# Kernel tuning notes

Measured on AMD Instinct MI355X. Metric: run time of the kernel, lower is better.

Reference implementation:

```python
import jax, jax.numpy as jnp
import numpy as np

N_NODES = 50000
N_EDGES = 640000
N_GRAPHS = 64
IN_DIM, HID, OUT_DIM = 128, 256, 4


def gcn_conv(x, src, dst, W, b, n_nodes):
    """PyG GCNConv: linear transform, then sym-normalized aggregation with self-loops."""
    h = x @ W  # [N, out]
    deg = jnp.zeros((n_nodes,), h.dtype).at[dst].add(1.0) + 1.0  # +1 self-loop
    dinv = jax.lax.rsqrt(deg)  # deg >= 1 always
    norm = dinv[src] * dinv[dst]  # [E]
    msg = h[src] * norm[:, None]  # [E, out]  gather + scale
    agg = jax.ops.segment_sum(msg, dst, num_segments=n_nodes)  # scatter-add
    agg = agg + h * (dinv * dinv)[:, None]  # self-loop contribution
    return agg + b


def global_mean_pool(x, batch, num_graphs):
    s = jax.ops.segment_sum(x, batch, num_segments=num_graphs)
    cnt = jax.ops.segment_sum(jnp.ones((x.shape[0],), x.dtype), batch, num_segments=num_graphs)
    return s / jnp.clip(cnt, 1.0)[:, None]


def setup_inputs() -> dict:
    key = jax.random.key(0)
    ks = jax.random.split(key, 8)
    x = jax.random.normal(ks[0], (N_NODES, IN_DIM), jnp.float32)
    src = jax.random.randint(ks[1], (N_EDGES,), 0, N_NODES, jnp.int64 if jax.config.jax_enable_x64 else jnp.int32)
    dst = jax.random.randint(ks[2], (N_EDGES,), 0, N_NODES, src.dtype)
    batch = jnp.sort(jax.random.randint(ks[3], (N_NODES,), 0, N_GRAPHS, src.dtype))
    W1 = jax.random.normal(ks[4], (IN_DIM, HID), jnp.float32) * (1.0 / np.sqrt(IN_DIM))
    b1 = jnp.zeros((HID,), jnp.float32)
    W2 = jax.random.normal(ks[5], (HID, HID // 2), jnp.float32) * (1.0 / np.sqrt(HID))
    b2 = jnp.zeros((HID // 2,), jnp.float32)
    Wfc = jax.random.normal(ks[6], (HID // 2, OUT_DIM), jnp.float32) * (1.0 / np.sqrt(HID // 2))
    bfc = jnp.zeros((OUT_DIM,), jnp.float32)
    return {"x": x, "src": src, "dst": dst, "batch": batch,
            "W1": W1, "b1": b1, "W2": W2, "b2": b2, "Wfc": Wfc, "bfc": bfc}


def reference(x, src, dst, batch, W1, b1, W2, b2, Wfc, bfc):
    n = x.shape[0]
    h = jax.nn.relu(gcn_conv(x, src, dst, W1, b1, n))   # dropout is identity at inference
    h = jax.nn.relu(gcn_conv(h, src, dst, W2, b2, n))
    g = global_mean_pool(h, batch, N_GRAPHS)            # [G, HID//2]
    return g @ Wfc + bfc                                # [G, OUT_DIM]
```

## Files before the change

### kernel.cpp

```cpp
#include <hip/hip_runtime.h>


constexpr int IN_DIM  = 128;
constexpr int HID     = 256;
constexpr int HID2    = 128;
constexpr int OUT_DIM = 4;
constexpr int NGRAPH  = 64;

typedef __attribute__((ext_vector_type(8))) short bf16x8;
typedef __attribute__((ext_vector_type(4))) float f32x4;

__device__ __forceinline__ short f2bf(float f) {
    union { float f; unsigned u; } v; v.f = f;
    unsigned r = v.u + 0x7fff + ((v.u >> 16) & 1);
    return (short)(r >> 16);
}
__device__ __forceinline__ float bf2f(short s) {
    union { unsigned u; float f; } v; v.u = ((unsigned)(unsigned short)s) << 16;
    return v.f;
}


__global__ void wprep_all_kernel(const float* __restrict__ W1, short* __restrict__ W1fh,
                                 short* __restrict__ W1fl,
                                 const float* __restrict__ W2, short* __restrict__ W2fh,
                                 short* __restrict__ W2fl,
                                 int* __restrict__ count, float* __restrict__ pool, int N) {
    int i = blockIdx.x * blockDim.x + threadIdx.x;
    if (i < IN_DIM * HID) {
        int slab = i >> 9, lane = (i >> 3) & 63, e = i & 7;
        int c4 = slab >> 2, ks = slab & 3;
        int col = c4 * 16 + (lane & 15);
        int k   = ks * 32 + (lane >> 4) * 8 + e;
        float w = W1[k * HID + col];
        short h = f2bf(w);
        W1fh[i] = h;
        W1fl[i] = f2bf(w - bf2f(h));
    }
    if (i < HID * HID2) {
        int slab = i >> 9, lane = (i >> 3) & 63, e = i & 7;
        int c4 = slab >> 3, ks = slab & 7;
        int col = c4 * 16 + (lane & 15);
        int k   = ks * 32 + (lane >> 4) * 8 + e;
        float w = W2[k * HID2 + col];
        short h = f2bf(w);
        W2fh[i] = h;
        W2fl[i] = f2bf(w - bf2f(h));
    }
    if (i < N) count[i] = 0;
    if (i < NGRAPH * HID2) pool[i] = 0.f;
}


__global__ void hist_kernel(const int* __restrict__ dst, int* __restrict__ count,
                            ushort* __restrict__ rank, int E) {
    int i = blockIdx.x * blockDim.x + threadIdx.x;
    if (i < E) rank[i] = (ushort)atomicAdd(&count[dst[i]], 1);
}

__global__ void scan1_kernel(const int* __restrict__ count, int* __restrict__ bsums, int N) {
    __shared__ int s[256];
    int t = threadIdx.x, i = blockIdx.x * 256 + t;
    int v = (i < N) ? count[i] : 0;
    s[t] = v; __syncthreads();
    for (int o = 1; o < 256; o <<= 1) {
        int x = (t >= o) ? s[t - o] : 0;
        __syncthreads(); s[t] += x; __syncthreads();
    }
    if (t == 255) bsums[blockIdx.x] = s[255];
}

__global__ void scan3_kernel(const int* __restrict__ count, const int* __restrict__ bsums,
                             int* __restrict__ rowptr, float* __restrict__ dinv,
                             int N, int E, int nb) {
    __shared__ int sb[256];
    __shared__ int s[256];
    int t = threadIdx.x, i = blockIdx.x * 256 + t;
    int bv = (t < nb) ? bsums[t] : 0;
    sb[t] = bv; __syncthreads();
    for (int o = 1; o < 256; o <<= 1) {
        int x = (t >= o) ? sb[t - o] : 0;
        __syncthreads(); sb[t] += x; __syncthreads();
    }
    int myex = (blockIdx.x == 0) ? 0 : sb[blockIdx.x - 1];
    int v = (i < N) ? count[i] : 0;
    s[t] = v; __syncthreads();
    for (int o = 1; o < 256; o <<= 1) {
        int x = (t >= o) ? s[t - o] : 0;
        __syncthreads(); s[t] += x; __syncthreads();
    }
    if (i < N) {
        rowptr[i] = myex + s[t] - v;
        dinv[i] = rsqrtf((float)v + 1.0f);
        if (i == 0) rowptr[N] = E;
    }
}

__global__ void scatter_scale_kernel(const int* __restrict__ src, const int* __restrict__ dst,
                                     const ushort* __restrict__ rank,
                                     const int* __restrict__ rowptr, ushort* __restrict__ csr,
                                     const float* __restrict__ x, const float* __restrict__ dinv,
                                     ushort* __restrict__ xb, int E, int total2) {
    int i = blockIdx.x * blockDim.x + threadIdx.x;
    if (i < E) {
        int p = rowptr[dst[i]] + (int)rank[i];
        csr[p] = (ushort)src[i];
    }
    if (i < total2) {
        float d = dinv[i >> 6];
        float2 v = ((const float2*)x)[i];
        ushort2 o;
        o.x = (ushort)f2bf(v.x * d);
        o.y = (ushort)f2bf(v.y * d);
        ((ushort2*)xb)[i] = o;
    }
}


__launch_bounds__(256, 2)
__global__ void mlp_fused_kernel(const short* __restrict__ A,
                                 const short* __restrict__ W1h, const short* __restrict__ W1l,
                                 const float* __restrict__ b1,
                                 const short* __restrict__ W2h, const short* __restrict__ W2l,
                                 const float* __restrict__ dinv,
                                 short* __restrict__ Cb, int M) {
    __shared__ __align__(16) short L[12288 + 6144];
    short* A1 = L;
    short* A0 = L + 12288;
    __shared__ float dinv_s[48];

    const int tid  = threadIdx.x;
    const int w    = tid >> 6;
    const int lane = tid & 63;
    const int l15  = lane & 15;
    const int kq8  = (lane >> 4) * 8;

    bf16x8 wh1[4][4], wl1[4][4];
#pragma unroll
    for (int ks = 0; ks < 4; ++ks)
#pragma unroll
        for (int n = 0; n < 4; ++n) {
            int slab = ((w * 4 + n) * 4 + ks) * 512;
            wh1[ks][n] = *(const bf16x8*)(W1h + slab + lane * 8);
            wl1[ks][n] = *(const bf16x8*)(W1l + slab + lane * 8);
        }

#pragma unroll 1
    for (int t = 0; t < 2; ++t) {
        const int row0 = (blockIdx.x * 2 + t) * 48;

        {
            bf16x8 stg[3];
#pragma unroll
            for (int j = 0; j < 3; ++j) {
                int s = w * 3 + j;
                int m = s >> 2, ks = s & 3;
                int rr = row0 + m * 16 + l15; if (rr >= M) rr = M - 1;
                stg[j] = *(const bf16x8*)(A + (size_t)rr * IN_DIM + ks * 32 + kq8);
            }
#pragma unroll
            for (int j = 0; j < 3; ++j)
                *(bf16x8*)&A0[(w * 3 + j) * 512 + lane * 8] = stg[j];
        }
        if (tid < 48) { int r = row0 + tid; dinv_s[tid] = dinv[r < M ? r : M - 1]; }
        __syncthreads();

        f32x4 acc1[3][4];
#pragma unroll
        for (int m = 0; m < 3; ++m)
#pragma unroll
            for (int n = 0; n < 4; ++n) acc1[m][n] = f32x4{0.f, 0.f, 0.f, 0.f};

#pragma unroll
        for (int ks = 0; ks < 4; ++ks) {
            bf16x8 af[3];
#pragma unroll
            for (int m = 0; m < 3; ++m) af[m] = *(const bf16x8*)&A0[(m * 4 + ks) * 512 + lane * 8];
#pragma unroll
            for (int m = 0; m < 3; ++m)
#pragma unroll
                for (int n = 0; n < 4; ++n) {
                    acc1[m][n] = __builtin_amdgcn_mfma_f32_16x16x32_bf16(af[m], wh1[ks][n], acc1[m][n], 0, 0, 0);
                    acc1[m][n] = __builtin_amdgcn_mfma_f32_16x16x32_bf16(af[m], wl1[ks][n], acc1[m][n], 0, 0, 0);
                }
        }

#pragma unroll
        for (int n = 0; n < 4; ++n) {
            int c  = w * 64 + n * 16 + l15;
            float bv = b1[c];
            int kst = c >> 5;
            int q  = (c >> 3) & 3;
            int e  = c & 7;
#pragma unroll
            for (int m = 0; m < 3; ++m)
#pragma unroll
                for (int r4 = 0; r4 < 4; ++r4) {
                    int rl = (lane >> 4) * 4 + r4;
                    int d  = rl + 16 * q;
                    float v = fmaxf(acc1[m][n][r4] + bv, 0.f);
                    A1[(m * 8 + kst) * 512 + d * 8 + e] = f2bf(v);
                }
        }

        bf16x8 wh2[8][2], wl2[8][2];
#pragma unroll
        for (int ks = 0; ks < 8; ++ks)
#pragma unroll
            for (int n = 0; n < 2; ++n) {
                int slab = ((w * 2 + n) * 8 + ks) * 512;
                wh2[ks][n] = *(const bf16x8*)(W2h + slab + lane * 8);
                wl2[ks][n] = *(const bf16x8*)(W2l + slab + lane * 8);
            }
        __syncthreads();

        f32x4 acc2[3][2];
#pragma unroll
        for (int m = 0; m < 3; ++m)
#pragma unroll
            for (int n = 0; n < 2; ++n) acc2[m][n] = f32x4{0.f, 0.f, 0.f, 0.f};

#pragma unroll
        for (int ks = 0; ks < 8; ++ks) {
            bf16x8 af[3];
#pragma unroll
            for (int m = 0; m < 3; ++m) af[m] = *(const bf16x8*)&A1[(m * 8 + ks) * 512 + lane * 8];
#pragma unroll
            for (int m = 0; m < 3; ++m)
#pragma unroll
                for (int n = 0; n < 2; ++n) {
                    acc2[m][n] = __builtin_amdgcn_mfma_f32_16x16x32_bf16(af[m], wh2[ks][n], acc2[m][n], 0, 0, 0);
                    acc2[m][n] = __builtin_amdgcn_mfma_f32_16x16x32_bf16(af[m], wl2[ks][n], acc2[m][n], 0, 0, 0);
                }
        }
        __syncthreads();

        short* T = A1;
#pragma unroll
        for (int n = 0; n < 2; ++n) {
            int c = w * 32 + n * 16 + l15;
#pragma unroll
            for (int m = 0; m < 3; ++m)
#pragma unroll
                for (int r4 = 0; r4 < 4; ++r4) {
                    int r = m * 16 + (lane >> 4) * 4 + r4;
                    T[r * 132 + c] = f2bf(acc2[m][n][r4] * dinv_s[r]);
                }
        }
        __syncthreads();
#pragma unroll
        for (int it = 0; it < 3; ++it) {
            int chunk = it * 256 + tid;
            int lr = chunk >> 4;
            int lc = (chunk & 15) * 8;
            int gr = row0 + lr;
            if (gr < M)
                *(bf16x8*)(Cb + (size_t)gr * HID2 + lc) = *(const bf16x8*)&T[lr * 132 + lc];
        }
        __syncthreads();
    }
}


template <bool POOL>
__launch_bounds__(256)
__global__ void agg_group_kernel(const ushort* __restrict__ hb, const float* __restrict__ dinv,
                                 const int* __restrict__ rowptr, const ushort* __restrict__ csr,
                                 const float* __restrict__ bias,
                                 short* __restrict__ oh,
                                 const int* __restrict__ batch, float* __restrict__ pool,
                                 int N) {
    __shared__ float pacc[16][128];
    __shared__ int   sgid[16];

    const int tid  = threadIdx.x;
    const int li   = tid & 15;
    const int nib  = tid >> 4;
    const int node = blockIdx.x * 16 + nib;
    const bool valid = node < N;
    if (!POOL && !valid) return;
    const int cw = valid ? node : N - 1;

    const int lo = rowptr[cw], hi = rowptr[cw + 1];
    const float dd = dinv[cw];

    float a[8];
    {
        bf16x8 sv = *(const bf16x8*)(hb + ((size_t)cw << 7) + (li << 3));
#pragma unroll
        for (int d = 0; d < 8; ++d) a[d] = bf2f(sv[d]);
    }

    const ushort* hsl = hb + (li << 3);

    for (int base = lo; base < hi; base += 16) {
        int cnt = min(16, hi - base);
        int sidx = (int)csr[base + (li < cnt ? li : cnt - 1)];
        bf16x8 p[8], q[8];
#pragma unroll
        for (int u = 0; u < 8; ++u) {
            int s = __shfl(sidx, u < cnt ? u : cnt - 1, 16);
            p[u] = *(const bf16x8*)(hsl + ((size_t)s << 7));
        }
#pragma unroll
        for (int u = 0; u < 8; ++u) {
            int e = 8 + u;
            int s = __shfl(sidx, e < cnt ? e : cnt - 1, 16);
            q[u] = *(const bf16x8*)(hsl + ((size_t)s << 7));
        }
#pragma unroll
        for (int u = 0; u < 8; ++u) {
            bool v = u < cnt;
#pragma unroll
            for (int d = 0; d < 8; ++d) a[d] += v ? bf2f(p[u][d]) : 0.f;
        }
#pragma unroll
        for (int u = 0; u < 8; ++u) {
            bool v = 8 + u < cnt;
#pragma unroll
            for (int d = 0; d < 8; ++d) a[d] += v ? bf2f(q[u][d]) : 0.f;
        }
    }

#pragma unroll
    for (int d = 0; d < 8; ++d) a[d] *= dd;

    if (!POOL) {
        if (valid) {
            bf16x8 o;
#pragma unroll
            for (int d = 0; d < 8; ++d) o[d] = f2bf(a[d]);
            *(bf16x8*)&oh[(size_t)node * 128 + li * 8] = o;
        }
        return;
    }

    {
        float4 b0 = ((const float4*)bias)[li * 2];
        float4 b1 = ((const float4*)bias)[li * 2 + 1];
        a[0] = fmaxf(a[0] + b0.x, 0.f); a[1] = fmaxf(a[1] + b0.y, 0.f);
        a[2] = fmaxf(a[2] + b0.z, 0.f); a[3] = fmaxf(a[3] + b0.w, 0.f);
        a[4] = fmaxf(a[4] + b1.x, 0.f); a[5] = fmaxf(a[5] + b1.y, 0.f);
        a[6] = fmaxf(a[6] + b1.z, 0.f); a[7] = fmaxf(a[7] + b1.w, 0.f);
    }
    if (li == 0) sgid[nib] = valid ? batch[node] : -1;
#pragma unroll
    for (int d = 0; d < 8; ++d) pacc[nib][li * 8 + d] = a[d];
    __syncthreads();
    if (tid < 128) {
        int c = tid;
        int cur = sgid[0];
        float run = 0.f;
#pragma unroll 1
        for (int w = 0; w < 16; ++w) {
            int gi = sgid[w];
            if (gi < 0) break;
            if (gi != cur) { atomicAdd(&pool[cur * HID2 + c], run); run = 0.f; cur = gi; }
            run += pacc[w][c];
        }
        atomicAdd(&pool[cur * HID2 + c], run);
    }
}


__device__ __forceinline__ int lower_bound_i(const int* __restrict__ a, int n, int key) {
    int lo = 0, hi = n;
    while (lo < hi) {
        int mid = (lo + hi) >> 1;
        if (a[mid] < key) lo = mid + 1; else hi = mid;
    }
    return lo;
}

__global__ void fc_kernel(const float* __restrict__ pool, const int* __restrict__ batch,
                          const float* __restrict__ Wfc, const float* __restrict__ bfc,
                          float* __restrict__ out, int N) {
    int t = threadIdx.x;
    int g = t >> 2, o = t & 3;
    int lo = lower_bound_i(batch, N, g);
    int hi = lower_bound_i(batch, N, g + 1);
    float acc = 0.f;
#pragma unroll 8
    for (int c = 0; c < HID2; ++c)
        acc = fmaf(pool[g * HID2 + c], Wfc[c * OUT_DIM + o], acc);
    float inv = 1.0f / fmaxf((float)(hi - lo), 1.0f);
    out[g * OUT_DIM + o] = acc * inv + bfc[o];
}

extern "C" void kernel_launch(void* const* d_in, const int* in_sizes, int n_in,
                              void* d_out, int out_size, void* d_ws, size_t ws_size,
                              hipStream_t stream) {
    const float* x   = (const float*)d_in[0];
    const int* src   = (const int*)d_in[1];
    const int* dst   = (const int*)d_in[2];
    const int* batch = (const int*)d_in[3];
    const float* W1  = (const float*)d_in[4];
    const float* b1  = (const float*)d_in[5];
    const float* W2  = (const float*)d_in[6];
    const float* b2  = (const float*)d_in[7];
    const float* Wfc = (const float*)d_in[8];
    const float* bfc = (const float*)d_in[9];
    float* out = (float*)d_out;

    const int N = in_sizes[0] / IN_DIM;
    const int E = in_sizes[1];
    const int NB = (N + 255) / 256;
    const int GA = (N + 15) / 16;
    const int GM = (N + 95) / 96;

    char* ws = (char*)d_ws;
    size_t off = 0;
    auto alloc = [&](size_t bytes) {
        char* p = ws + off;
        off = (off + bytes + 255) & ~(size_t)255;
        return p;
    };
    float*  dinv   = (float*) alloc((size_t)N * 4);
    int*    count  = (int*)   alloc((size_t)N * 4);
    int*    rowptr = (int*)   alloc((size_t)(N + 1) * 4);
    int*    bsums  = (int*)   alloc(256 * 4);
    ushort* rank   = (ushort*)alloc((size_t)E * 2);
    ushort* csr    = (ushort*)alloc((size_t)E * 2);
    short*  W1th   = (short*) alloc((size_t)IN_DIM * HID * 2);
    short*  W1tl   = (short*) alloc((size_t)IN_DIM * HID * 2);
    short*  W2th   = (short*) alloc((size_t)HID * HID2 * 2);
    short*  W2tl   = (short*) alloc((size_t)HID * HID2 * 2);
    ushort* xb     = (ushort*)alloc((size_t)N * IN_DIM * 2);
    short*  axb    = (short*) alloc((size_t)N * IN_DIM * 2);
    float*  pool   = (float*) alloc((size_t)NGRAPH * HID2 * 4);
    ushort* h2b = xb;

    wprep_all_kernel<<<(max(IN_DIM * HID, N) + 255) / 256, 256, 0, stream>>>(
        W1, W1th, W1tl, W2, W2th, W2tl, count, pool, N);

    hist_kernel<<<(E + 255) / 256, 256, 0, stream>>>(dst, count, rank, E);
    scan1_kernel<<<NB, 256, 0, stream>>>(count, bsums, N);
    scan3_kernel<<<NB, 256, 0, stream>>>(count, bsums, rowptr, dinv, N, E, NB);
    scatter_scale_kernel<<<(N * 64 + 255) / 256, 256, 0, stream>>>(
        src, dst, rank, rowptr, csr, x, dinv, xb, E, N * 64);

    agg_group_kernel<false><<<GA, 256, 0, stream>>>(
        xb, dinv, rowptr, csr, nullptr, axb, nullptr, nullptr, N);

    mlp_fused_kernel<<<GM, 256, 0, stream>>>(
        axb, W1th, W1tl, b1, W2th, W2tl, dinv, (short*)h2b, N);

    agg_group_kernel<true><<<GA, 256, 0, stream>>>(
        h2b, dinv, rowptr, csr, b2, nullptr, batch, pool, N);

    fc_kernel<<<1, NGRAPH * OUT_DIM, 0, stream>>>(pool, batch, Wfc, bfc, out, N);
}
```

Before: 269.0 us.

## Stream MLP weights per k-step instead of register-caching, one tile per block

The fused MLP kernel stops preloading all W1/W2 hi/lo fragments into registers. It now loads each k-slice's weight fragments from global memory inside the MFMA loop, and each block processes a single 48-row tile instead of two. Launch bounds rise to 4 blocks per CU and the grid doubles, which cuts register pressure and raises occupancy. In exchange, weights are re-read from L2/L1 on every k-step with no reuse across tiles, and those loads sit directly in front of the MFMAs.

```diff
diff --git a/kernel.cpp b/kernel.cpp
--- a/kernel.cpp
+++ b/kernel.cpp
@@ -117,7 +117,7 @@
 }
 
 
-__launch_bounds__(256, 2)
+__launch_bounds__(256, 4)
 __global__ void mlp_fused_kernel(const short* __restrict__ A,
                                  const short* __restrict__ W1h, const short* __restrict__ W1l,
                                  const float* __restrict__ b1,
@@ -134,130 +134,117 @@
     const int lane = tid & 63;
     const int l15  = lane & 15;
     const int kq8  = (lane >> 4) * 8;
-
-    bf16x8 wh1[4][4], wl1[4][4];
-#pragma unroll
-    for (int ks = 0; ks < 4; ++ks)
+    const int row0 = blockIdx.x * 48;
+
+    {
+        bf16x8 stg[3];
+#pragma unroll
+        for (int j = 0; j < 3; ++j) {
+            int s = w * 3 + j;
+            int m = s >> 2, ks = s & 3;
+            int rr = row0 + m * 16 + l15; if (rr >= M) rr = M - 1;
+            stg[j] = *(const bf16x8*)(A + (size_t)rr * IN_DIM + ks * 32 + kq8);
+        }
+#pragma unroll
+        for (int j = 0; j < 3; ++j)
+            *(bf16x8*)&A0[(w * 3 + j) * 512 + lane * 8] = stg[j];
+    }
+    if (tid < 48) { int r = row0 + tid; dinv_s[tid] = dinv[r < M ? r : M - 1]; }
+    __syncthreads();
+
+    f32x4 acc1[3][4];
+#pragma unroll
+    for (int m = 0; m < 3; ++m)
+#pragma unroll
+        for (int n = 0; n < 4; ++n) acc1[m][n] = f32x4{0.f, 0.f, 0.f, 0.f};
+
+#pragma unroll
+    for (int ks = 0; ks < 4; ++ks) {
+        bf16x8 af[3], bh[4], bl[4];
+#pragma unroll
+        for (int m = 0; m < 3; ++m) af[m] = *(const bf16x8*)&A0[(m * 4 + ks) * 512 + lane * 8];
 #pragma unroll
         for (int n = 0; n < 4; ++n) {
             int slab = ((w * 4 + n) * 4 + ks) * 512;
-            wh1[ks][n] = *(const bf16x8*)(W1h + slab + lane * 8);
-            wl1[ks][n] = *(const bf16x8*)(W1l + slab + lane * 8);
-        }
-
-#pragma unroll 1
-    for (int t = 0; t < 2; ++t) {
-        const int row0 = (blockIdx.x * 2 + t) * 48;
-
-        {
-            bf16x8 stg[3];
-#pragma unroll
-            for (int j = 0; j < 3; ++j) {
-                int s = w * 3 + j;
-                int m = s >> 2, ks = s & 3;
-                int rr = row0 + m * 16 + l15; if (rr >= M) rr = M - 1;
-                stg[j] = *(const bf16x8*)(A + (size_t)rr * IN_DIM + ks * 32 + kq8);
+            bh[n] = *(const bf16x8*)(W1h + slab + lane * 8);
+            bl[n] = *(const bf16x8*)(W1l + slab + lane * 8);
+        }
+#pragma unroll
+        for (int m = 0; m < 3; ++m)
+#pragma unroll
+            for (int n = 0; n < 4; ++n) {
+                acc1[m][n] = __builtin_amdgcn_mfma_f32_16x16x32_bf16(af[m], bh[n], acc1[m][n], 0, 0, 0);
+                acc1[m][n] = __builtin_amdgcn_mfma_f32_16x16x32_bf16(af[m], bl[n], acc1[m][n], 0, 0, 0);
             }
-#pragma unroll
-            for (int j = 0; j < 3; ++j)
-                *(bf16x8*)&A0[(w * 3 + j) * 512 + lane * 8] = stg[j];
-        }
-        if (tid < 48) { int r = row0 + tid; dinv_s[tid] = dinv[r < M ? r : M - 1]; }
-        __syncthreads();
-
-        f32x4 acc1[3][4];
+    }
+
+#pragma unroll
+    for (int n = 0; n < 4; ++n) {
+        int c  = w * 64 + n * 16 + l15;
+        float bv = b1[c];
+        int kst = c >> 5;
+        int q  = (c >> 3) & 3;
+        int e  = c & 7;
 #pragma unroll
         for (int m = 0; m < 3; ++m)
 #pragma unroll
-            for (int n = 0; n < 4; ++n) acc1[m][n] = f32x4{0.f, 0.f, 0.f, 0.f};
-
-#pragma unroll
-        for (int ks = 0; ks < 4; ++ks) {
-            bf16x8 af[3];
-#pragma unroll
-            for (int m = 0; m < 3; ++m) af[m] = *(const bf16x8*)&A0[(m * 4 + ks) * 512 + lane * 8];
-#pragma unroll
-            for (int m = 0; m < 3; ++m)
-#pragma unroll
-                for (int n = 0; n < 4; ++n) {
-                    acc1[m][n] = __builtin_amdgcn_mfma_f32_16x16x32_bf16(af[m], wh1[ks][n], acc1[m][n], 0, 0, 0);
-                    acc1[m][n] = __builtin_amdgcn_mfma_f32_16x16x32_bf16(af[m], wl1[ks][n], acc1[m][n], 0, 0, 0);
-                }
-        }
-
-#pragma unroll
-        for (int n = 0; n < 4; ++n) {
-            int c  = w * 64 + n * 16 + l15;
-            float bv = b1[c];
-            int kst = c >> 5;
-            int q  = (c >> 3) & 3;
-            int e  = c & 7;
-#pragma unroll
-            for (int m = 0; m < 3; ++m)
-#pragma unroll
-                for (int r4 = 0; r4 < 4; ++r4) {
-                    int rl = (lane >> 4) * 4 + r4;
-                    int d  = rl + 16 * q;
-                    float v = fmaxf(acc1[m][n][r4] + bv, 0.f);
-                    A1[(m * 8 + kst) * 512 + d * 8 + e] = f2bf(v);
-                }
-        }
-
-        bf16x8 wh2[8][2], wl2[8][2];
-#pragma unroll
-        for (int ks = 0; ks < 8; ++ks)
+            for (int r4 = 0; r4 < 4; ++r4) {
+                int rl = (lane >> 4) * 4 + r4;
+                int d  = rl + 16 * q;
+                float v = fmaxf(acc1[m][n][r4] + bv, 0.f);
+                A1[(m * 8 + kst) * 512 + d * 8 + e] = f2bf(v);
+            }
+    }
+    __syncthreads();
+
+    f32x4 acc2[3][2];
+#pragma unroll
+    for (int m = 0; m < 3; ++m)
+#pragma unroll
+        for (int n = 0; n < 2; ++n) acc2[m][n] = f32x4{0.f, 0.f, 0.f, 0.f};
+
+#pragma unroll
+    for (int ks = 0; ks < 8; ++ks) {
+        bf16x8 af[3], bh[2], bl[2];
+#pragma unroll
+        for (int m = 0; m < 3; ++m) af[m] = *(const bf16x8*)&A1[(m * 8 + ks) * 512 + lane * 8];
+#pragma unroll
+        for (int n = 0; n < 2; ++n) {
+            int slab = ((w * 2 + n) * 8 + ks) * 512;
+            bh[n] = *(const bf16x8*)(W2h + slab + lane * 8);
+            bl[n] = *(const bf16x8*)(W2l + slab + lane * 8);
+        }
+#pragma unroll
+        for (int m = 0; m < 3; ++m)
 #pragma unroll
             for (int n = 0; n < 2; ++n) {
-                int slab = ((w * 2 + n) * 8 + ks) * 512;
-                wh2[ks][n] = *(const bf16x8*)(W2h + slab + lane * 8);
-                wl2[ks][n] = *(const bf16x8*)(W2l + slab + lane * 8);
+                acc2[m][n] = __builtin_amdgcn_mfma_f32_16x16x32_bf16(af[m], bh[n], acc2[m][n], 0, 0, 0);
+                acc2[m][n] = __builtin_amdgcn_mfma_f32_16x16x32_bf16(af[m], bl[n], acc2[m][n], 0, 0, 0);
             }
-        __syncthreads();
-
-        f32x4 acc2[3][2];
+    }
+    __syncthreads();
+
+    short* T = A1;
+#pragma unroll
+    for (int n = 0; n < 2; ++n) {
+        int c = w * 32 + n * 16 + l15;
 #pragma unroll
         for (int m = 0; m < 3; ++m)
 #pragma unroll
-            for (int n = 0; n < 2; ++n) acc2[m][n] = f32x4{0.f, 0.f, 0.f, 0.f};
-
-#pragma unroll
-        for (int ks = 0; ks < 8; ++ks) {
-            bf16x8 af[3];
-#pragma unroll
-            for (int m = 0; m < 3; ++m) af[m] = *(const bf16x8*)&A1[(m * 8 + ks) * 512 + lane * 8];
-#pragma unroll
-            for (int m = 0; m < 3; ++m)
-#pragma unroll
-                for (int n = 0; n < 2; ++n) {
-                    acc2[m][n] = __builtin_amdgcn_mfma_f32_16x16x32_bf16(af[m], wh2[ks][n], acc2[m][n], 0, 0, 0);
-                    acc2[m][n] = __builtin_amdgcn_mfma_f32_16x16x32_bf16(af[m], wl2[ks][n], acc2[m][n], 0, 0, 0);
-                }
-        }
-        __syncthreads();
-
-        short* T = A1;
-#pragma unroll
-        for (int n = 0; n < 2; ++n) {
-            int c = w * 32 + n * 16 + l15;
-#pragma unroll
-            for (int m = 0; m < 3; ++m)
-#pragma unroll
-                for (int r4 = 0; r4 < 4; ++r4) {
-                    int r = m * 16 + (lane >> 4) * 4 + r4;
-                    T[r * 132 + c] = f2bf(acc2[m][n][r4] * dinv_s[r]);
-                }
-        }
-        __syncthreads();
-#pragma unroll
-        for (int it = 0; it < 3; ++it) {
-            int chunk = it * 256 + tid;
-            int lr = chunk >> 4;
-            int lc = (chunk & 15) * 8;
-            int gr = row0 + lr;
-            if (gr < M)
-                *(bf16x8*)(Cb + (size_t)gr * HID2 + lc) = *(const bf16x8*)&T[lr * 132 + lc];
-        }
-        __syncthreads();
+            for (int r4 = 0; r4 < 4; ++r4) {
+                int r = m * 16 + (lane >> 4) * 4 + r4;
+                T[r * 132 + c] = f2bf(acc2[m][n][r4] * dinv_s[r]);
+            }
+    }
+    __syncthreads();
+#pragma unroll
+    for (int it = 0; it < 3; ++it) {
+        int chunk = it * 256 + tid;
+        int lr = chunk >> 4;
+        int lc = (chunk & 15) * 8;
+        int gr = row0 + lr;
+        if (gr < M)
+            *(bf16x8*)(Cb + (size_t)gr * HID2 + lc) = *(const bf16x8*)&T[lr * 132 + lc];
     }
 }
 
@@ -406,7 +393,7 @@
     const int E = in_sizes[1];
     const int NB = (N + 255) / 256;
     const int GA = (N + 15) / 16;
-    const int GM = (N + 95) / 96;
+    const int GM = (N + 47) / 48;
 
     char* ws = (char*)d_ws;
     size_t off = 0;
```

Result: faster. 225.7 us (-16.1%).
